# Performance work log

Hardware: AMD Instinct MI355X
Metric: run time of the kernel (lower is better)

## Reference

```python
import jax, jax.numpy as jnp
import numpy as np

B, N, HID = 1, 2048, 1024
H, WK, WV = 16, 64, 64
DH = HID // H  # 64


def setup_inputs() -> dict:
    key = jax.random.key(0)
    ks = jax.random.split(key, 10)
    s = 0.02
    return {
        "hidden_states": jax.random.normal(ks[0], (B, N, HID), jnp.float32),
        "attention_mask": jnp.ones((B, N), jnp.float32),
        "Wq": jax.random.normal(ks[1], (HID, HID), jnp.float32) * s,
        "bq": jnp.zeros((HID,), jnp.float32),
        "Wk": jax.random.normal(ks[2], (HID, HID), jnp.float32) * s,
        "bk": jnp.zeros((HID,), jnp.float32),
        "Wv": jax.random.normal(ks[3], (HID, HID), jnp.float32) * s,
        "bv": jnp.zeros((HID,), jnp.float32),
        # Conv1D(2*WK+1, DH, bias=False): weight [nx=DH, nf=2*WK+1]
        "W_rel_k": jax.random.normal(ks[4], (DH, 2 * WK + 1), jnp.float32) * s,
        # relative_pos_val: [2*WV+1, DH]
        "W_rel_v": jax.random.normal(ks[5], (2 * WV + 1, DH), jnp.float32) * s,
    }


def _attention(hidden_states, attention_mask, Wq, bq, Wk, bk, Wv, bv, W_rel_k, W_rel_v):
    b, n, _ = hidden_states.shape

    def heads(x):  # [B,N,HID] -> [B,H,N,DH]
        return x.reshape(b, n, H, DH).transpose(0, 2, 1, 3)

    q = heads(hidden_states @ Wq + bq)
    k = heads(hidden_states @ Wk + bk)
    v = heads(hidden_states @ Wv + bv)

    scores = jnp.einsum("bhid,bhjd->bhij", q, k)  # [B,H,N,N]

    # --- relative-position key bias: bias[i, j] = q_i . w_{j-i+WK} for |j-i|<=WK ---
    a_k = jnp.einsum("bhid,dw->bhiw", q, W_rel_k)  # [B,H,N,2*WK+1]
    rows = jnp.arange(n)
    slot = rows[None, :] - rows[:, None] + WK       # [N,N] relative slot j-i+WK
    valid_k = (slot >= 0) & (slot <= 2 * WK)
    bias = a_k[:, :, rows[:, None], jnp.clip(slot, 0, 2 * WK)]  # [B,H,N,N]
    scores = scores + jnp.where(valid_k, bias, 0.0)

    scores = scores / np.float32(np.sqrt(DH))  # temperature == 1.0

    # extended attention mask: (1 - mask) * dtype_min added to scores
    ext = (1.0 - attention_mask)[:, None, None, :] * jnp.finfo(scores.dtype).min
    scores = scores + ext

    probs = jax.nn.softmax(scores, axis=-1)  # [B,H,N,N]

    ctx = jnp.einsum("bhij,bhjd->bhid", probs, v)  # [B,H,N,DH]

    # --- relative-position value: band[i, r] = probs[i, i-WV+r]; ctx += band @ W_rel_v ---
    offs = jnp.arange(2 * WV + 1)
    kpos = rows[:, None] - WV + offs[None, :]       # [N, 2*WV+1] absolute key position
    valid_v = (kpos >= 0) & (kpos < n)
    band = probs[:, :, rows[:, None], jnp.clip(kpos, 0, n - 1)]  # [B,H,N,2*WV+1]
    band = jnp.where(valid_v, band, 0.0)
    ctx = ctx + jnp.einsum("bhiw,wd->bhid", band, W_rel_v)

    # merge heads -> [B,N,HID]
    return ctx.transpose(0, 2, 1, 3).reshape(b, n, HID)


def reference(hidden_states, attention_mask, Wq, bq, Wk, bk, Wv, bv, W_rel_k, W_rel_v):
    return _attention(hidden_states, attention_mask, Wq, bq, Wk, bk, Wv, bv, W_rel_k, W_rel_v)
```

## Files before the change

### kernel.cpp

```cpp
#include <hip/hip_runtime.h>
#include <hip/hip_bf16.h>

#define NSEQ 2048
#define HIDDIM 1024
#define NH 16
#define DHEAD 64
#define NW 129
#define AKS 132

typedef float          f32x4 __attribute__((ext_vector_type(4)));
typedef _Float16       f16x4 __attribute__((ext_vector_type(4)));
typedef _Float16       f16x8 __attribute__((ext_vector_type(8)));
typedef unsigned short u16x8 __attribute__((ext_vector_type(8)));
typedef unsigned short u16;

__device__ __forceinline__ float b2f(u16 u){ return __uint_as_float(((unsigned)u) << 16); }
__device__ __forceinline__ float ld_any(const void* p, long idx, int flag){
  return flag ? b2f(((const u16*)p)[idx]) : ((const float*)p)[idx];
}
__device__ __forceinline__ int dtype_flag(const void* mask){
  return (((const unsigned*)mask)[0] == 0x3F800000u) ? 0 : 1;
}

#define GLOAD_LDS16(gp, lp) \
  __builtin_amdgcn_global_load_lds((const __attribute__((address_space(1))) unsigned int*)(gp), \
                                   (__attribute__((address_space(3))) unsigned int*)(lp), 16, 0, 0)

static const size_t OFF_Q    = 0;
static const size_t OFF_K    = (size_t)4  << 20;
static const size_t OFF_VT   = (size_t)8  << 20;
static const size_t OFF_WT   = (size_t)12 << 20;
static const size_t OFF_AK   = (size_t)18 << 20;
static const size_t OFF_M    = OFF_AK + (size_t)NH * NSEQ * AKS * 4;
static const size_t OFF_L    = OFF_M + (size_t)2 * NH * NSEQ * 4;
static const size_t OFF_CTXP = OFF_L + (size_t)2 * NH * NSEQ * 4;
static const size_t OFF_HSF  = OFF_CTXP + (size_t)2 * NSEQ * HIDDIM * 4;
static const size_t OFF_BIAS = OFF_HSF + (size_t)NSEQ * HIDDIM * 2;
static const size_t OFF_EXT  = OFF_BIAS + 3 * 1024 * 4;
static const size_t OFF_WRKT = OFF_EXT + (size_t)NSEQ * 4;
static const size_t OFF_WRVT = OFF_WRKT + (size_t)144 * 72 * 2;

__global__ void cvt_all_kernel(const void* __restrict__ hs, const void* __restrict__ mask,
                               const void* __restrict__ bq, const void* __restrict__ bk,
                               const void* __restrict__ bv, const void* __restrict__ wrk,
                               const void* __restrict__ wrv,
                               _Float16* __restrict__ hsf, float* __restrict__ biasf,
                               float* __restrict__ extf, _Float16* __restrict__ wrkT16,
                               _Float16* __restrict__ wrvT16){
  const int flag = dtype_flag(mask);
  const int b = blockIdx.x;
  if (b < 1024){
    const long base = (long)(b * 256 + threadIdx.x) * 8;
    f16x8 o;
    if (flag){
      u16x8 v = *(const u16x8*)((const u16*)hs + base);
#pragma unroll
      for (int e = 0; e < 8; e++) o[e] = (_Float16)b2f(v[e]);
    } else {
      f32x4 a = *(const f32x4*)((const float*)hs + base);
      f32x4 c = *(const f32x4*)((const float*)hs + base + 4);
#pragma unroll
      for (int e = 0; e < 4; e++){ o[e] = (_Float16)a[e]; o[4 + e] = (_Float16)c[e]; }
    }
    *(f16x8*)(hsf + base) = o;
    return;
  }
  const int idx = (b - 1024) * 256 + threadIdx.x;
  if (idx < 1024)            biasf[idx] = ld_any(bq, idx, flag);
  else if (idx < 2048)       biasf[idx] = ld_any(bk, idx - 1024, flag);
  else if (idx < 3072)       biasf[idx] = ld_any(bv, idx - 2048, flag);
  else if (idx < 5120)       extf[idx - 3072] = (1.f - ld_any(mask, idx - 3072, flag)) * -1.0e30f;
  else if (idx < 5120 + 144 * 72){
    int i2 = idx - 5120;
    int w = i2 / 72, d = i2 - w * 72;
    wrkT16[i2] = (w < NW && d < 64) ? (_Float16)ld_any(wrk, (long)d * NW + w, flag) : (_Float16)0.f;
  } else if (idx < 5120 + 144 * 72 + 64 * 144){
    int i3 = idx - (5120 + 144 * 72);
    int d = i3 / 144, w = i3 - d * 144;
    wrvT16[i3] = (w < NW) ? (_Float16)ld_any(wrv, (long)w * 64 + d, flag) : (_Float16)0.f;
  }
}

__global__ void wtrans_kernel(const void* __restrict__ Wq, const void* __restrict__ Wk,
                              const void* __restrict__ Wv, const void* __restrict__ mask,
                              _Float16* __restrict__ Wt){
  __shared__ __attribute__((aligned(16))) _Float16 tile[64][65];
  const int flag = dtype_flag(mask);
  const int z = blockIdx.z;
  const void* src = (z == 0) ? Wq : ((z == 1) ? Wk : Wv);
  _Float16* dst = Wt + (size_t)z * 1024 * 1024;
  const int o0 = blockIdx.x * 64, k0 = blockIdx.y * 64;
  const int t = threadIdx.x;
#pragma unroll
  for (int c = 0; c < 2; c++){
    int idx = t + 256 * c;
    int r = idx >> 3, c8 = (idx & 7) * 8;
    long off = (long)(k0 + r) * 1024 + o0 + c8;
    if (flag){
      u16x8 v = *(const u16x8*)((const u16*)src + off);
#pragma unroll
      for (int e = 0; e < 8; e++) tile[r][c8 + e] = (_Float16)b2f(v[e]);
    } else {
      f32x4 a = *(const f32x4*)((const float*)src + off);
      f32x4 b = *(const f32x4*)((const float*)src + off + 4);
#pragma unroll
      for (int e = 0; e < 4; e++){ tile[r][c8 + e] = (_Float16)a[e]; tile[r][c8 + 4 + e] = (_Float16)b[e]; }
    }
  }
  __syncthreads();
#pragma unroll
  for (int c = 0; c < 2; c++){
    int idx = t + 256 * c;
    int orow = idx >> 3, k8 = (idx & 7) * 8;
    f16x8 v;
#pragma unroll
    for (int e = 0; e < 8; e++) v[e] = tile[k8 + e][orow];
    *(f16x8*)(dst + (size_t)(o0 + orow) * 1024 + k0 + k8) = v;
  }
}

__launch_bounds__(256, 3)
__global__ void qkv_kernel(const _Float16* __restrict__ hsf, const _Float16* __restrict__ Wt,
                           const float* __restrict__ biasf,
                           _Float16* __restrict__ Qf, _Float16* __restrict__ Kf,
                           _Float16* __restrict__ Vtf){
  __shared__ __attribute__((aligned(16))) _Float16 As[2 * 64 * 32];
  __shared__ __attribute__((aligned(16))) _Float16 Bs[2 * 128 * 32];
  const int z = blockIdx.z;
  const _Float16* Wz = Wt + (size_t)z * 1024 * 1024;
  const int o0 = blockIdx.x * 128, m0 = blockIdx.y * 64;
  const int t = threadIdx.x, lane = t & 63, wave = t >> 6;
  const int wm = wave >> 1, wn = wave & 1;
  const int q = lane >> 4, ln = lane & 15;

  auto stage = [&](int nb, int k0){
    {
      const int row = t >> 2, chunk = t & 3;
      const _Float16* gA = hsf + (size_t)(m0 + row) * 1024 + k0 + chunk * 8;
      _Float16* lA = (_Float16*)As + nb * 2048 + (wave << 9);
      GLOAD_LDS16(gA, lA);
    }
#pragma unroll
    for (int p = 0; p < 2; p++){
      const int idx = p * 256 + t;
      const int row = idx >> 2, chunk = idx & 3;
      const _Float16* gB = Wz + (size_t)(o0 + row) * 1024 + k0 + chunk * 8;
      _Float16* lB = (_Float16*)Bs + nb * 4096 + ((p * 4 + wave) << 9);
      GLOAD_LDS16(gB, lB);
    }
  };

  f32x4 acc[2][4];
#pragma unroll
  for (int a = 0; a < 2; a++)
#pragma unroll
    for (int b = 0; b < 4; b++) acc[a][b] = (f32x4){0.f, 0.f, 0.f, 0.f};

  stage(0, 0);
  __syncthreads();
  int cur = 0;
  for (int k0 = 0; k0 < 1024; k0 += 32){
    if (k0 + 32 < 1024) stage(cur ^ 1, k0 + 32);
    const _Float16* Ac = (const _Float16*)As + cur * 2048;
    const _Float16* Bc = (const _Float16*)Bs + cur * 4096;
    f16x8 af[2], bf[4];
#pragma unroll
    for (int mt = 0; mt < 2; mt++) af[mt] = *(const f16x8*)&Ac[(wm * 32 + mt * 16 + ln) * 32 + q * 8];
#pragma unroll
    for (int nt = 0; nt < 4; nt++) bf[nt] = *(const f16x8*)&Bc[(wn * 64 + nt * 16 + ln) * 32 + q * 8];
    __builtin_amdgcn_s_setprio(1);
#pragma unroll
    for (int mt = 0; mt < 2; mt++)
#pragma unroll
      for (int nt = 0; nt < 4; nt++)
        acc[mt][nt] = __builtin_amdgcn_mfma_f32_16x16x32_f16(af[mt], bf[nt], acc[mt][nt], 0, 0, 0);
    __builtin_amdgcn_s_setprio(0);
    __syncthreads();
    cur ^= 1;
  }
  const float sc = (z == 0) ? 0.125f : 1.0f;
#pragma unroll
  for (int nt = 0; nt < 4; nt++){
    int o = o0 + wn * 64 + nt * 16 + ln;
    float bval = biasf[z * 1024 + o];
    int hh = o >> 6, dd = o & 63;
#pragma unroll
    for (int mt = 0; mt < 2; mt++){
      int nb = m0 + wm * 32 + mt * 16 + q * 4;
      if (z == 2){
        f16x4 pk;
#pragma unroll
        for (int r = 0; r < 4; r++) pk[r] = (_Float16)(acc[mt][nt][r] + bval);
        *(f16x4*)(Vtf + (size_t)(hh * 64 + dd) * 2048 + nb) = pk;
      } else {
        _Float16* dstp = (z == 0) ? Qf : Kf;
#pragma unroll
        for (int r = 0; r < 4; r++)
          dstp[(size_t)(hh * 2048 + nb + r) * 64 + dd] = (_Float16)((acc[mt][nt][r] + bval) * sc);
      }
    }
  }
}

__launch_bounds__(256, 2)
__global__ void ak_kernel(const _Float16* __restrict__ Qf, const _Float16* __restrict__ wrkT16,
                          float* __restrict__ ak){
  __shared__ __attribute__((aligned(16))) _Float16 WrkT[144 * 72];
  const int h = blockIdx.y;
  const int i0 = blockIdx.x * 128;
  const int t = threadIdx.x, lane = t & 63, wave = t >> 6;
  const int q = lane >> 4, ln = lane & 15;
  {
    const f16x8* srcv = (const f16x8*)wrkT16;
    f16x8* dstv = (f16x8*)WrkT;
#pragma unroll
    for (int c = 0; c < 6; c++){
      int v = c * 256 + t;
      if (v < 144 * 72 / 8) dstv[v] = srcv[v];
    }
  }
  __syncthreads();
  f16x8 afr[2][2];
#pragma unroll
  for (int mt = 0; mt < 2; mt++){
    int row = i0 + wave * 32 + mt * 16 + ln;
#pragma unroll
    for (int ks = 0; ks < 2; ks++)
      afr[mt][ks] = *(const f16x8*)(Qf + (size_t)(h * 2048 + row) * 64 + ks * 32 + q * 8);
  }
  f32x4 acc[2][9];
#pragma unroll
  for (int a = 0; a < 2; a++)
#pragma unroll
    for (int b = 0; b < 9; b++) acc[a][b] = (f32x4){0.f, 0.f, 0.f, 0.f};
#pragma unroll
  for (int nt = 0; nt < 9; nt++){
    f16x8 bfr0 = *(const f16x8*)&WrkT[(nt * 16 + ln) * 72 + q * 8];
    f16x8 bfr1 = *(const f16x8*)&WrkT[(nt * 16 + ln) * 72 + 32 + q * 8];
#pragma unroll
    for (int mt = 0; mt < 2; mt++){
      acc[mt][nt] = __builtin_amdgcn_mfma_f32_16x16x32_f16(afr[mt][0], bfr0, acc[mt][nt], 0, 0, 0);
      acc[mt][nt] = __builtin_amdgcn_mfma_f32_16x16x32_f16(afr[mt][1], bfr1, acc[mt][nt], 0, 0, 0);
    }
  }
#pragma unroll
  for (int nt = 0; nt < 9; nt++){
    int w = nt * 16 + ln;
    if (w > 128) continue;
#pragma unroll
    for (int mt = 0; mt < 2; mt++){
      int ib = i0 + wave * 32 + mt * 16 + q * 4;
#pragma unroll
      for (int r = 0; r < 4; r++)
        ak[(size_t)(h * 2048 + ib + r) * AKS + w] = acc[mt][nt][r];
    }
  }
}

__launch_bounds__(256, 4)
__global__ void flash_kernel(const float* __restrict__ extf,
                             const _Float16* __restrict__ Qf, const _Float16* __restrict__ Kf,
                             const _Float16* __restrict__ Vtf, float* akm,
                             float* __restrict__ ctxpart, float* __restrict__ mws,
                             float* __restrict__ lws){
  __shared__ __attribute__((aligned(16))) _Float16 Ks[2 * 64 * 64];
  __shared__ __attribute__((aligned(16))) _Float16 Vts[2 * 64 * 64];
  __shared__ __attribute__((aligned(16))) float Exts[1024];
  __shared__ int eflags[4];
  const int h = blockIdx.x, qt = blockIdx.y, jh = blockIdx.z;
  const int t = threadIdx.x, lane = t & 63, wave = t >> 6;
  const int q = lane >> 4, ln = lane & 15;
  const int ibase = qt * 64 + wave * 16;
  const int i = ibase + ln;
  const int jb = jh * 1024;

  auto stageK = [&](int nb, int jn){
#pragma unroll
    for (int p = 0; p < 2; p++){
      const int g = p * 256 + t;
      const int row = g >> 3, slot = g & 7;
      const int col8 = slot ^ (row & 7);
      GLOAD_LDS16(Kf + (((size_t)(h * 2048 + jn + row)) << 6) + (col8 << 3),
                  (_Float16*)Ks + nb * 4096 + ((p * 4 + wave) << 9));
    }
  };
  auto stageV = [&](int nb, int jn){
#pragma unroll
    for (int p = 0; p < 2; p++){
      const int g = p * 256 + t;
      const int row = g >> 3, slot = g & 7;
      const int col8 = slot ^ (row & 7);
      GLOAD_LDS16(Vtf + (((size_t)(h * 64 + row)) << 11) + jn + (col8 << 3),
                  (_Float16*)Vts + nb * 4096 + ((p * 4 + wave) << 9));
    }
  };

  const int ds7 = ln & 7;
  const _Float16* kb0 = (const _Float16*)Ks + (ln << 6) + ((q ^ ds7) << 3);
  const _Float16* kb1 = (const _Float16*)Ks + (ln << 6) + (((q + 4) ^ ds7) << 3);
  const _Float16* vb0 = (const _Float16*)Vts + (ln << 6) + (((0 | (q >> 1)) ^ ds7) << 3) + ((q & 1) << 2);
  const _Float16* vb1 = (const _Float16*)Vts + (ln << 6) + (((2 | (q >> 1)) ^ ds7) << 3) + ((q & 1) << 2);
  const _Float16* vb2 = (const _Float16*)Vts + (ln << 6) + (((4 | (q >> 1)) ^ ds7) << 3) + ((q & 1) << 2);
  const _Float16* vb3 = (const _Float16*)Vts + (ln << 6) + (((6 | (q >> 1)) ^ ds7) << 3) + ((q & 1) << 2);

  f16x8 qfrag[2];
  {
    const _Float16* qrow = Qf + (size_t)(h * 2048 + i) * 64;
    qfrag[0] = *(const f16x8*)(qrow + q * 8);
    qfrag[1] = *(const f16x8*)(qrow + 32 + q * 8);
  }
  f32x4 accc[4];
#pragma unroll
  for (int dt = 0; dt < 4; dt++) accc[dt] = (f32x4){0.f, 0.f, 0.f, 0.f};
  float m_i = -1.0e30f, l_i = 0.f;
  float* akrow = akm + (size_t)(h * 2048 + i) * AKS;
  f32x4 s[4];

  auto qk = [&](int PK){
    __builtin_amdgcn_s_setprio(1);
#pragma unroll
    for (int mt = 0; mt < 4; mt++){
      f16x8 kf0 = *(const f16x8*)(kb0 + PK * 4096 + mt * 1024);
      f16x8 kf1 = *(const f16x8*)(kb1 + PK * 4096 + mt * 1024);
      f32x4 zz = (f32x4){0.f, 0.f, 0.f, 0.f};
      zz = __builtin_amdgcn_mfma_f32_16x16x32_f16(kf0, qfrag[0], zz, 0, 0, 0);
      zz = __builtin_amdgcn_mfma_f32_16x16x32_f16(kf1, qfrag[1], zz, 0, 0, 0);
      s[mt] = zz;
    }
    __builtin_amdgcn_s_setprio(0);
  };

  bool nz = false;
#pragma unroll
  for (int c = 0; c < 4; c++){
    float e = extf[jb + c * 256 + t];
    Exts[c * 256 + t] = e;
    nz |= (e != 0.f);
  }
  {
    unsigned long long bz = __ballot(nz);
    if (lane == 0) eflags[wave] = (bz != 0ull) ? 1 : 0;
  }
  stageK(0, jb);
  __syncthreads();
  const bool extNZ = (eflags[0] | eflags[1] | eflags[2] | eflags[3]) != 0;
  stageV(0, jb);
  stageK(1, jb + 64);
  qk(0);
  __syncthreads();

  auto body = [&](int t_, int PV_, int PK1, bool last){
    const int j0 = jb + t_ * 64;
    if (!last){
      stageV(PK1, j0 + 64);
      if (t_ < 14) stageK(PV_, j0 + 128);
    }
    const bool band = (j0 <= ibase + 79) && (j0 + 63 >= ibase - 64);
    if (band){
#pragma unroll
      for (int mt = 0; mt < 4; mt++){
        f32x4 ev = *(const f32x4*)&Exts[t_ * 64 + mt * 16 + (q << 2)];
#pragma unroll
        for (int r = 0; r < 4; r++){
          float x = s[mt][r];
          int w = j0 + mt * 16 + (q << 2) + r - i + 64;
          if ((unsigned)w <= 128u){
            x = x + akrow[w] + ev[r];
            akrow[w] = x;
          } else {
            x = x + ev[r];
          }
          s[mt][r] = x;
        }
      }
    } else if (extNZ){
#pragma unroll
      for (int mt = 0; mt < 4; mt++){
        f32x4 ev = *(const f32x4*)&Exts[t_ * 64 + mt * 16 + (q << 2)];
#pragma unroll
        for (int r = 0; r < 4; r++) s[mt][r] += ev[r];
      }
    }
    float a0 = fmaxf(fmaxf(s[0][0], s[0][1]), fmaxf(s[0][2], s[0][3]));
    float a1 = fmaxf(fmaxf(s[1][0], s[1][1]), fmaxf(s[1][2], s[1][3]));
    float a2 = fmaxf(fmaxf(s[2][0], s[2][1]), fmaxf(s[2][2], s[2][3]));
    float a3 = fmaxf(fmaxf(s[3][0], s[3][1]), fmaxf(s[3][2], s[3][3]));
    float tmax = fmaxf(fmaxf(a0, a1), fmaxf(a2, a3));
    tmax = fmaxf(tmax, __shfl_xor(tmax, 16, 64));
    tmax = fmaxf(tmax, __shfl_xor(tmax, 32, 64));
    float mnew = fmaxf(m_i, tmax);
    if (!__all(tmax <= m_i)){
      float alpha = __expf(m_i - mnew);
      l_i *= alpha;
#pragma unroll
      for (int dt = 0; dt < 4; dt++)
#pragma unroll
        for (int r = 0; r < 4; r++) accc[dt][r] *= alpha;
    }
    m_i = mnew;
    float ps[4][4];
#pragma unroll
    for (int mt = 0; mt < 4; mt++)
#pragma unroll
      for (int r = 0; r < 4; r++) ps[mt][r] = __expf(s[mt][r] - mnew);
    f16x4 pf[4];
#pragma unroll
    for (int mt = 0; mt < 4; mt++)
#pragma unroll
      for (int r = 0; r < 4; r++) pf[mt][r] = (_Float16)ps[mt][r];
    float t0 = (ps[0][0] + ps[0][1]) + (ps[0][2] + ps[0][3]);
    float t1 = (ps[1][0] + ps[1][1]) + (ps[1][2] + ps[1][3]);
    float t2 = (ps[2][0] + ps[2][1]) + (ps[2][2] + ps[2][3]);
    float t3 = (ps[3][0] + ps[3][1]) + (ps[3][2] + ps[3][3]);
    float tsum = (t0 + t1) + (t2 + t3);
    tsum += __shfl_xor(tsum, 16, 64);
    tsum += __shfl_xor(tsum, 32, 64);
    l_i += tsum;
    if (!last) qk(PK1);
    __builtin_amdgcn_s_setprio(1);
#pragma unroll
    for (int dt = 0; dt < 4; dt++){
      f16x4 vf0 = *(const f16x4*)(vb0 + PV_ * 4096 + dt * 1024);
      f16x4 vf1 = *(const f16x4*)(vb1 + PV_ * 4096 + dt * 1024);
      f16x4 vf2 = *(const f16x4*)(vb2 + PV_ * 4096 + dt * 1024);
      f16x4 vf3 = *(const f16x4*)(vb3 + PV_ * 4096 + dt * 1024);
      accc[dt] = __builtin_amdgcn_mfma_f32_16x16x16f16(vf0, pf[0], accc[dt], 0, 0, 0);
      accc[dt] = __builtin_amdgcn_mfma_f32_16x16x16f16(vf1, pf[1], accc[dt], 0, 0, 0);
      accc[dt] = __builtin_amdgcn_mfma_f32_16x16x16f16(vf2, pf[2], accc[dt], 0, 0, 0);
      accc[dt] = __builtin_amdgcn_mfma_f32_16x16x16f16(vf3, pf[3], accc[dt], 0, 0, 0);
    }
    __builtin_amdgcn_s_setprio(0);
    __syncthreads();
  };

  for (int tt = 0; tt < 8; tt++){
    body(2 * tt,     0, 1, false);
    body(2 * tt + 1, 1, 0, tt == 7);
  }

  float* cdst = ctxpart + (size_t)jh * NSEQ * HIDDIM;
#pragma unroll
  for (int dt = 0; dt < 4; dt++)
    *(f32x4*)(cdst + (size_t)i * 1024 + h * 64 + dt * 16 + q * 4) = accc[dt];
  if (q == 0){
    mws[jh * NH * NSEQ + h * 2048 + i] = m_i;
    lws[jh * NH * NSEQ + h * 2048 + i] = l_i;
  }
}

__launch_bounds__(256, 2)
__global__ void finish_kernel(const float* __restrict__ sband, const float* __restrict__ mws,
                              const float* __restrict__ lws, const _Float16* __restrict__ wrvT16,
                              const float* __restrict__ ctxpart, float* __restrict__ out){
  __shared__ __attribute__((aligned(16))) _Float16 WrvT[64 * 144];
  __shared__ __attribute__((aligned(16))) _Float16 pT[144 * 72];
  __shared__ __attribute__((aligned(16))) float sM[64], sIL[64], sC0[64], sC1[64];
  const int qt = blockIdx.x, h = blockIdx.y;
  const int i0 = qt * 64;
  const int t = threadIdx.x, lane = t & 63, wave = t >> 6;
  const int q = lane >> 4, ln = lane & 15;
  {
    const f16x8* srcv = (const f16x8*)wrvT16;
    f16x8* dstv = (f16x8*)WrvT;
#pragma unroll
    for (int c = 0; c < 5; c++){
      int v = c * 256 + t;
      if (v < 64 * 144 / 8) dstv[v] = srcv[v];
    }
  }
  if (t < 64){
    int i = i0 + t;
    float m0 = mws[h * 2048 + i],            m1 = mws[NH * NSEQ + h * 2048 + i];
    float l0 = lws[h * 2048 + i],            l1 = lws[NH * NSEQ + h * 2048 + i];
    float M = fmaxf(m0, m1);
    float a0 = __expf(m0 - M), a1 = __expf(m1 - M);
    float L = a0 * l0 + a1 * l1;
    float iL = 1.f / L;
    sM[t] = M; sIL[t] = iL; sC0[t] = a0 * iL; sC1[t] = a1 * iL;
  }
  __syncthreads();
  for (int ii = 0; ii < 16; ii++){
    int il = wave * 16 + ii;
    float Mv = sM[il], ILv = sIL[il];
    const float* srow = sband + (size_t)(h * 2048 + i0 + il) * AKS;
#pragma unroll
    for (int c = 0; c < 3; c++){
      int w = lane + 64 * c;
      if (w < 144){
        float p = (w < NW) ? __expf(srow[w] - Mv) * ILv : 0.f;
        pT[w * 72 + il] = (_Float16)p;
      }
    }
  }
  __syncthreads();
  f32x4 acc[4];
#pragma unroll
  for (int mt = 0; mt < 4; mt++) acc[mt] = (f32x4){0.f, 0.f, 0.f, 0.f};
#pragma unroll
  for (int ks = 0; ks < 9; ks++){
    f16x4 bfr;
#pragma unroll
    for (int j = 0; j < 4; j++) bfr[j] = pT[(ks * 16 + q * 4 + j) * 72 + wave * 16 + ln];
#pragma unroll
    for (int mt = 0; mt < 4; mt++){
      f16x4 afr = *(const f16x4*)&WrvT[(mt * 16 + ln) * 144 + ks * 16 + q * 4];
      acc[mt] = __builtin_amdgcn_mfma_f32_16x16x16f16(afr, bfr, acc[mt], 0, 0, 0);
    }
  }
  const int i = i0 + wave * 16 + ln;
  const float c0 = sC0[wave * 16 + ln], c1 = sC1[wave * 16 + ln];
  const float* p0 = ctxpart;
  const float* p1 = ctxpart + (size_t)NSEQ * HIDDIM;
#pragma unroll
  for (int mt = 0; mt < 4; mt++){
    size_t off = (size_t)i * 1024 + h * 64 + mt * 16 + q * 4;
    f32x4 A0 = *(const f32x4*)(p0 + off);
    f32x4 A1 = *(const f32x4*)(p1 + off);
    f32x4 o4;
#pragma unroll
    for (int r = 0; r < 4; r++) o4[r] = c0 * A0[r] + c1 * A1[r] + acc[mt][r];
    *(f32x4*)(out + off) = o4;
  }
}

extern "C" void kernel_launch(void* const* d_in, const int* in_sizes, int n_in,
                              void* d_out, int out_size, void* d_ws, size_t ws_size,
                              hipStream_t stream){
  const void* hs   = d_in[0];
  const void* mask = d_in[1];
  const void* Wq   = d_in[2];
  const void* bq   = d_in[3];
  const void* Wk   = d_in[4];
  const void* bk   = d_in[5];
  const void* Wv   = d_in[6];
  const void* bv   = d_in[7];
  const void* Wrk  = d_in[8];
  const void* Wrv  = d_in[9];
  float* out = (float*)d_out;

  char* ws = (char*)d_ws;
  _Float16* Qf    = (_Float16*)(ws + OFF_Q);
  _Float16* Kf    = (_Float16*)(ws + OFF_K);
  _Float16* Vtf   = (_Float16*)(ws + OFF_VT);
  _Float16* Wt    = (_Float16*)(ws + OFF_WT);
  float*    akp   = (float*)   (ws + OFF_AK);
  float*    mp    = (float*)   (ws + OFF_M);
  float*    lp    = (float*)   (ws + OFF_L);
  float*    ctxp  = (float*)   (ws + OFF_CTXP);
  _Float16* hsf   = (_Float16*)(ws + OFF_HSF);
  float*    biasf = (float*)   (ws + OFF_BIAS);
  float*    extf  = (float*)   (ws + OFF_EXT);
  _Float16* wrkT16= (_Float16*)(ws + OFF_WRKT);
  _Float16* wrvT16= (_Float16*)(ws + OFF_WRVT);

  cvt_all_kernel  <<<dim3(1121),       256, 0, stream>>>(hs, mask, bq, bk, bv, Wrk, Wrv,
                                                         hsf, biasf, extf, wrkT16, wrvT16);
  wtrans_kernel   <<<dim3(16, 16, 3),  256, 0, stream>>>(Wq, Wk, Wv, mask, Wt);
  qkv_kernel      <<<dim3(8, 32, 3),   256, 0, stream>>>(hsf, Wt, biasf, Qf, Kf, Vtf);
  ak_kernel       <<<dim3(16, 16),     256, 0, stream>>>(Qf, wrkT16, akp);
  flash_kernel    <<<dim3(16, 32, 2),  256, 0, stream>>>(extf, Qf, Kf, Vtf, akp, ctxp, mp, lp);
  finish_kernel   <<<dim3(32, 16),     256, 0, stream>>>(akp, mp, lp, wrvT16, ctxp, out);
}
```

Before: 186.9 us.

## Retile QKV GEMM with swizzled LDS, split ak blocks, rotate flash key order

The QKV projection GEMM moves to 512-thread blocks with 128x128 tiles, a K step of 64, and XOR-swizzled LDS layouts. This should raise operand reuse and cut LDS bank conflicts. The ak kernel now uses 64-row blocks, one M tile per wave, which doubles the grid. The flash kernel rotates the order in which each block visits its key tiles by a per-block phase, spreading L2/HBM traffic and the band-processing work across blocks. The cost is higher LDS use per QKV block and more ak blocks, and the band-mask logic must stay correct under the permuted order.

```diff
diff --git a/kernel.cpp b/kernel.cpp
--- a/kernel.cpp
+++ b/kernel.cpp
@@ -119,74 +119,79 @@
   }
 }
 
-__launch_bounds__(256, 3)
+__launch_bounds__(512, 4)
 __global__ void qkv_kernel(const _Float16* __restrict__ hsf, const _Float16* __restrict__ Wt,
                            const float* __restrict__ biasf,
                            _Float16* __restrict__ Qf, _Float16* __restrict__ Kf,
                            _Float16* __restrict__ Vtf){
-  __shared__ __attribute__((aligned(16))) _Float16 As[2 * 64 * 32];
-  __shared__ __attribute__((aligned(16))) _Float16 Bs[2 * 128 * 32];
+  __shared__ __attribute__((aligned(16))) _Float16 As[2 * 128 * 64];
+  __shared__ __attribute__((aligned(16))) _Float16 Bs[2 * 128 * 64];
   const int z = blockIdx.z;
   const _Float16* Wz = Wt + (size_t)z * 1024 * 1024;
-  const int o0 = blockIdx.x * 128, m0 = blockIdx.y * 64;
+  const int o0 = blockIdx.x * 128, m0 = blockIdx.y * 128;
   const int t = threadIdx.x, lane = t & 63, wave = t >> 6;
-  const int wm = wave >> 1, wn = wave & 1;
+  const int wm = wave >> 2, wn = wave & 3;
   const int q = lane >> 4, ln = lane & 15;
 
   auto stage = [&](int nb, int k0){
-    {
-      const int row = t >> 2, chunk = t & 3;
-      const _Float16* gA = hsf + (size_t)(m0 + row) * 1024 + k0 + chunk * 8;
-      _Float16* lA = (_Float16*)As + nb * 2048 + (wave << 9);
-      GLOAD_LDS16(gA, lA);
-    }
 #pragma unroll
     for (int p = 0; p < 2; p++){
-      const int idx = p * 256 + t;
-      const int row = idx >> 2, chunk = idx & 3;
-      const _Float16* gB = Wz + (size_t)(o0 + row) * 1024 + k0 + chunk * 8;
-      _Float16* lB = (_Float16*)Bs + nb * 4096 + ((p * 4 + wave) << 9);
-      GLOAD_LDS16(gB, lB);
+      const int g = p * 512 + t;
+      const int row = g >> 3, slot = g & 7;
+      const int c8 = slot ^ (row & 7);
+      GLOAD_LDS16(hsf + (size_t)(m0 + row) * 1024 + k0 + (c8 << 3),
+                  (_Float16*)As + nb * 8192 + ((p * 8 + wave) << 9));
+      GLOAD_LDS16(Wz + (size_t)(o0 + row) * 1024 + k0 + (c8 << 3),
+                  (_Float16*)Bs + nb * 8192 + ((p * 8 + wave) << 9));
     }
   };
 
-  f32x4 acc[2][4];
-#pragma unroll
-  for (int a = 0; a < 2; a++)
-#pragma unroll
-    for (int b = 0; b < 4; b++) acc[a][b] = (f32x4){0.f, 0.f, 0.f, 0.f};
+  f32x4 acc[4][2];
+#pragma unroll
+  for (int a = 0; a < 4; a++)
+#pragma unroll
+    for (int b = 0; b < 2; b++) acc[a][b] = (f32x4){0.f, 0.f, 0.f, 0.f};
 
   stage(0, 0);
   __syncthreads();
   int cur = 0;
-  for (int k0 = 0; k0 < 1024; k0 += 32){
-    if (k0 + 32 < 1024) stage(cur ^ 1, k0 + 32);
-    const _Float16* Ac = (const _Float16*)As + cur * 2048;
-    const _Float16* Bc = (const _Float16*)Bs + cur * 4096;
-    f16x8 af[2], bf[4];
-#pragma unroll
-    for (int mt = 0; mt < 2; mt++) af[mt] = *(const f16x8*)&Ac[(wm * 32 + mt * 16 + ln) * 32 + q * 8];
-#pragma unroll
-    for (int nt = 0; nt < 4; nt++) bf[nt] = *(const f16x8*)&Bc[(wn * 64 + nt * 16 + ln) * 32 + q * 8];
+  for (int k0 = 0; k0 < 1024; k0 += 64){
+    if (k0 + 64 < 1024) stage(cur ^ 1, k0 + 64);
+    const _Float16* Ac = (const _Float16*)As + cur * 8192;
+    const _Float16* Bc = (const _Float16*)Bs + cur * 8192;
     __builtin_amdgcn_s_setprio(1);
 #pragma unroll
-    for (int mt = 0; mt < 2; mt++)
-#pragma unroll
-      for (int nt = 0; nt < 4; nt++)
-        acc[mt][nt] = __builtin_amdgcn_mfma_f32_16x16x32_f16(af[mt], bf[nt], acc[mt][nt], 0, 0, 0);
+    for (int ks = 0; ks < 2; ks++){
+      f16x8 af[4], bf[2];
+#pragma unroll
+      for (int mt = 0; mt < 4; mt++){
+        int row = wm * 64 + mt * 16 + ln;
+        af[mt] = *(const f16x8*)&Ac[(row << 6) + (((ks * 4 + q) ^ (row & 7)) << 3)];
+      }
+#pragma unroll
+      for (int nt = 0; nt < 2; nt++){
+        int row = wn * 32 + nt * 16 + ln;
+        bf[nt] = *(const f16x8*)&Bc[(row << 6) + (((ks * 4 + q) ^ (row & 7)) << 3)];
+      }
+#pragma unroll
+      for (int mt = 0; mt < 4; mt++)
+#pragma unroll
+        for (int nt = 0; nt < 2; nt++)
+          acc[mt][nt] = __builtin_amdgcn_mfma_f32_16x16x32_f16(af[mt], bf[nt], acc[mt][nt], 0, 0, 0);
+    }
     __builtin_amdgcn_s_setprio(0);
     __syncthreads();
     cur ^= 1;
   }
   const float sc = (z == 0) ? 0.125f : 1.0f;
 #pragma unroll
-  for (int nt = 0; nt < 4; nt++){
-    int o = o0 + wn * 64 + nt * 16 + ln;
+  for (int nt = 0; nt < 2; nt++){
+    int o = o0 + wn * 32 + nt * 16 + ln;
     float bval = biasf[z * 1024 + o];
     int hh = o >> 6, dd = o & 63;
 #pragma unroll
-    for (int mt = 0; mt < 2; mt++){
-      int nb = m0 + wm * 32 + mt * 16 + q * 4;
+    for (int mt = 0; mt < 4; mt++){
+      int nb = m0 + wm * 64 + mt * 16 + q * 4;
       if (z == 2){
         f16x4 pk;
 #pragma unroll
@@ -207,7 +212,7 @@
                           float* __restrict__ ak){
   __shared__ __attribute__((aligned(16))) _Float16 WrkT[144 * 72];
   const int h = blockIdx.y;
-  const int i0 = blockIdx.x * 128;
+  const int i0 = blockIdx.x * 64;
   const int t = threadIdx.x, lane = t & 63, wave = t >> 6;
   const int q = lane >> 4, ln = lane & 15;
   {
@@ -220,40 +225,29 @@
     }
   }
   __syncthreads();
-  f16x8 afr[2][2];
-#pragma unroll
-  for (int mt = 0; mt < 2; mt++){
-    int row = i0 + wave * 32 + mt * 16 + ln;
-#pragma unroll
-    for (int ks = 0; ks < 2; ks++)
-      afr[mt][ks] = *(const f16x8*)(Qf + (size_t)(h * 2048 + row) * 64 + ks * 32 + q * 8);
-  }
-  f32x4 acc[2][9];
-#pragma unroll
-  for (int a = 0; a < 2; a++)
-#pragma unroll
-    for (int b = 0; b < 9; b++) acc[a][b] = (f32x4){0.f, 0.f, 0.f, 0.f};
+  const int row = i0 + wave * 16 + ln;
+  f16x8 afr[2];
+#pragma unroll
+  for (int ks = 0; ks < 2; ks++)
+    afr[ks] = *(const f16x8*)(Qf + (size_t)(h * 2048 + row) * 64 + ks * 32 + q * 8);
+  f32x4 acc[9];
+#pragma unroll
+  for (int b = 0; b < 9; b++) acc[b] = (f32x4){0.f, 0.f, 0.f, 0.f};
 #pragma unroll
   for (int nt = 0; nt < 9; nt++){
     f16x8 bfr0 = *(const f16x8*)&WrkT[(nt * 16 + ln) * 72 + q * 8];
     f16x8 bfr1 = *(const f16x8*)&WrkT[(nt * 16 + ln) * 72 + 32 + q * 8];
-#pragma unroll
-    for (int mt = 0; mt < 2; mt++){
-      acc[mt][nt] = __builtin_amdgcn_mfma_f32_16x16x32_f16(afr[mt][0], bfr0, acc[mt][nt], 0, 0, 0);
-      acc[mt][nt] = __builtin_amdgcn_mfma_f32_16x16x32_f16(afr[mt][1], bfr1, acc[mt][nt], 0, 0, 0);
-    }
+    acc[nt] = __builtin_amdgcn_mfma_f32_16x16x32_f16(afr[0], bfr0, acc[nt], 0, 0, 0);
+    acc[nt] = __builtin_amdgcn_mfma_f32_16x16x32_f16(afr[1], bfr1, acc[nt], 0, 0, 0);
   }
 #pragma unroll
   for (int nt = 0; nt < 9; nt++){
     int w = nt * 16 + ln;
     if (w > 128) continue;
-#pragma unroll
-    for (int mt = 0; mt < 2; mt++){
-      int ib = i0 + wave * 32 + mt * 16 + q * 4;
-#pragma unroll
-      for (int r = 0; r < 4; r++)
-        ak[(size_t)(h * 2048 + ib + r) * AKS + w] = acc[mt][nt][r];
-    }
+    int ib = i0 + wave * 16 + q * 4;
+#pragma unroll
+    for (int r = 0; r < 4; r++)
+      ak[(size_t)(h * 2048 + ib + r) * AKS + w] = acc[nt][r];
   }
 }
 
@@ -273,6 +267,7 @@
   const int ibase = qt * 64 + wave * 16;
   const int i = ibase + ln;
   const int jb = jh * 1024;
+  const int phase = (h + 3 * qt + 8 * jh) & 15;
 
   auto stageK = [&](int nb, int jn){
 #pragma unroll
@@ -330,6 +325,8 @@
     __builtin_amdgcn_s_setprio(0);
   };
 
+  auto jof = [&](int x){ return jb + ((x + phase) & 15) * 64; };
+
   bool nz = false;
 #pragma unroll
   for (int c = 0; c < 4; c++){
@@ -341,25 +338,26 @@
     unsigned long long bz = __ballot(nz);
     if (lane == 0) eflags[wave] = (bz != 0ull) ? 1 : 0;
   }
-  stageK(0, jb);
+  stageK(0, jof(0));
   __syncthreads();
   const bool extNZ = (eflags[0] | eflags[1] | eflags[2] | eflags[3]) != 0;
-  stageV(0, jb);
-  stageK(1, jb + 64);
+  stageV(0, jof(0));
+  stageK(1, jof(1));
   qk(0);
   __syncthreads();
 
   auto body = [&](int t_, int PV_, int PK1, bool last){
-    const int j0 = jb + t_ * 64;
+    const int j0 = jof(t_);
     if (!last){
-      stageV(PK1, j0 + 64);
-      if (t_ < 14) stageK(PV_, j0 + 128);
+      stageV(PK1, jof(t_ + 1));
+      if (t_ < 14) stageK(PV_, jof(t_ + 2));
     }
     const bool band = (j0 <= ibase + 79) && (j0 + 63 >= ibase - 64);
+    const int je = (t_ + phase) & 15;
     if (band){
 #pragma unroll
       for (int mt = 0; mt < 4; mt++){
-        f32x4 ev = *(const f32x4*)&Exts[t_ * 64 + mt * 16 + (q << 2)];
+        f32x4 ev = *(const f32x4*)&Exts[je * 64 + mt * 16 + (q << 2)];
 #pragma unroll
         for (int r = 0; r < 4; r++){
           float x = s[mt][r];
@@ -376,7 +374,7 @@
     } else if (extNZ){
 #pragma unroll
       for (int mt = 0; mt < 4; mt++){
-        f32x4 ev = *(const f32x4*)&Exts[t_ * 64 + mt * 16 + (q << 2)];
+        f32x4 ev = *(const f32x4*)&Exts[je * 64 + mt * 16 + (q << 2)];
 #pragma unroll
         for (int r = 0; r < 4; r++) s[mt][r] += ev[r];
       }
@@ -556,8 +554,8 @@
   cvt_all_kernel  <<<dim3(1121),       256, 0, stream>>>(hs, mask, bq, bk, bv, Wrk, Wrv,
                                                          hsf, biasf, extf, wrkT16, wrvT16);
   wtrans_kernel   <<<dim3(16, 16, 3),  256, 0, stream>>>(Wq, Wk, Wv, mask, Wt);
-  qkv_kernel      <<<dim3(8, 32, 3),   256, 0, stream>>>(hsf, Wt, biasf, Qf, Kf, Vtf);
-  ak_kernel       <<<dim3(16, 16),     256, 0, stream>>>(Qf, wrkT16, akp);
+  qkv_kernel      <<<dim3(8, 16, 3),   512, 0, stream>>>(hsf, Wt, biasf, Qf, Kf, Vtf);
+  ak_kernel       <<<dim3(32, 16),     256, 0, stream>>>(Qf, wrkT16, akp);
   flash_kernel    <<<dim3(16, 32, 2),  256, 0, stream>>>(extf, Qf, Kf, Vtf, akp, ctxp, mp, lp);
   finish_kernel   <<<dim3(32, 16),     256, 0, stream>>>(akp, mp, lp, wrvT16, ctxp, out);
 }
```

After: 179.6 us. 3.9% less time.
